# Optimization experiments

Hardware: AMD Instinct MI355X
Metric: run time of the kernel (lower is better)

Reference implementation:

```python
import jax, jax.numpy as jnp
import numpy as np

BITS = 4
GROUPSIZE = 128
INF = 4096
OUTF = 4096
PACK = 32 // BITS  # 8 nibbles per int32


def _dequant(qweight, qzeros, scales):
    # qweight: [INF//PACK, OUTF] int32, qzeros: [n_groups, OUTF//PACK] int32
    shifts = (jnp.arange(PACK, dtype=jnp.int32) * BITS)
    # unpack weights: each int32 row holds PACK consecutive input rows
    w = (qweight[:, None, :] >> shifts[None, :, None]) & 15        # [512, 8, 4096]
    w = w.reshape(-1, GROUPSIZE, OUTF)                              # [n_groups, groupsize, OUTF]
    # unpack zeros: each int32 col holds PACK consecutive output cols
    z = ((qzeros[:, :, None] >> shifts[None, None, :]) & 15) + 1   # [n_groups, 512, 8]
    z = z.reshape(z.shape[0], 1, -1)                                # [n_groups, 1, OUTF]
    W = scales[:, None, :] * (w - z).astype(scales.dtype)           # per-group dequant
    return W.reshape(INF, OUTF)


def setup_inputs() -> dict:
    key = jax.random.key(0)
    k1, k2, k3, k4, k5 = jax.random.split(key, 5)
    x = jax.random.normal(k1, (8, 512, INF), dtype=jnp.float32)
    qweight = jax.random.randint(k2, (INF // PACK, OUTF), 0, 2147483647, dtype=jnp.int32)
    n_groups = INF // GROUPSIZE
    qzeros = jax.random.randint(k3, (n_groups, OUTF // PACK), 0, 2147483647, dtype=jnp.int32)
    scales = jax.random.uniform(k4, (n_groups, OUTF), dtype=jnp.float32) * 0.01 + 0.001
    bias = jax.random.normal(k5, (OUTF,), dtype=jnp.float32) * 0.01
    return {"x": x, "qweight": qweight, "qzeros": qzeros, "scales": scales, "bias": bias}


def reference(x, qweight, qzeros, scales, bias):
    W = _dequant(qweight, qzeros, scales)        # [INF, OUTF] fp32
    out = jnp.matmul(x, W.astype(x.dtype)) + bias
    return out
```

## Files before the change

kernel.cpp:

```cpp
#include <hip/hip_runtime.h>
#include <hip/hip_bf16.h>


#define K_DIM 4096
#define N_DIM 4096
#define M_DIM 4096
#define BM 128
#define BN 128
#define BK 64
#define NGROUPS 32

typedef __attribute__((ext_vector_type(8))) short s8v;
typedef __attribute__((ext_vector_type(4))) float f4v;
typedef __attribute__((ext_vector_type(4))) unsigned int u4v;
typedef __attribute__((ext_vector_type(2))) unsigned int u2v;
typedef __attribute__((ext_vector_type(4))) float float4v;

typedef __attribute__((address_space(3))) void LDSV;
typedef const __attribute__((address_space(1))) void GLBV;

__device__ __forceinline__ void glds16(const void* g, void* l) {
    __builtin_amdgcn_global_load_lds((GLBV*)g, (LDSV*)l, 16, 0, 0);
}

__device__ __forceinline__ unsigned int bf16rne(float f) {
    unsigned int b = __float_as_uint(f);
    return (b + 0x7FFFu + ((b >> 16) & 1u)) >> 16;
}

__global__ __launch_bounds__(256) void castx(const float* __restrict__ x,
                                             unsigned short* __restrict__ xh,
                                             int n4) {
    int i0 = blockIdx.x * 256 + threadIdx.x;
    int st = gridDim.x * 256;
    for (int i = i0; i < n4; i += st) {
        float4v v = ((const float4v*)x)[i];
        unsigned int h[4];
#pragma unroll
        for (int j = 0; j < 4; j++) {
            unsigned int b = __float_as_uint(v[j]);
            h[j] = (b + 0x7FFFu + ((b >> 16) & 1u)) & 0xFFFF0000u;
        }
        u2v o = {(h[0] >> 16) | h[1], (h[2] >> 16) | h[3]};
        ((u2v*)xh)[i] = o;
    }
}

__global__ __launch_bounds__(256) void dequantW(const int* __restrict__ qw,
                                                const int* __restrict__ qz,
                                                const float* __restrict__ scales,
                                                unsigned short* __restrict__ wt) {
    __shared__ __align__(16) unsigned short T[256 * 64];
    const int b = blockIdx.x;
    const int kkb = b & 63;
    const int nb = b >> 6;
    const int tid = threadIdx.x;
    const int n = nb * 256 + tid;
    const int g = kkb >> 1;
    const float s = scales[g * N_DIM + n];
    const int zp1 = ((qz[g * 512 + (n >> 3)] >> ((n & 7) * 4)) & 15) + 1;

    char* Tb = (char*)T;
#pragma unroll
    for (int r = 0; r < 8; r++) {
        const unsigned int q = (unsigned int)qw[(kkb * 8 + r) * N_DIM + n];
        unsigned int hw[8];
#pragma unroll
        for (int j = 0; j < 8; j++) {
            float v = s * (float)((int)((q >> (4 * j)) & 15u) - zp1);
            hw[j] = bf16rne(v);
        }
        u4v d = {hw[0] | (hw[1] << 16), hw[2] | (hw[3] << 16),
                 hw[4] | (hw[5] << 16), hw[6] | (hw[7] << 16)};
        *(u4v*)(Tb + tid * 128 + ((r * 16) ^ ((tid & 7) << 4))) = d;
    }
    __syncthreads();
#pragma unroll
    for (int p = 0; p < 8; p++) {
        const int nl = p * 32 + (tid >> 3);
        const int c = tid & 7;
        u4v d = *(const u4v*)(Tb + nl * 128 + ((c * 16) ^ ((nl & 7) << 4)));
        *(u4v*)(wt + (size_t)(nb * 256 + nl) * K_DIM + kkb * 64 + c * 8) = d;
    }
}

__global__ __launch_bounds__(256, 2) void gemm_q4(
    const unsigned short* __restrict__ xh, const unsigned short* __restrict__ wt,
    const float* __restrict__ bias, float* __restrict__ out) {
    __shared__ __align__(16) unsigned short A[2][BM * BK];
    __shared__ __align__(16) unsigned short B[2][BN * BK];

    const int tid = threadIdx.x;
    const int lane = tid & 63;
    const int wid = tid >> 6;

    const int bid = blockIdx.x;
    const int wg = ((bid & 7) << 7) + (bid >> 3);
    const int bm = (wg >> 5) << 7;
    const int bn = (wg & 31) << 7;

    const int wr = ((wid >> 1) & 1) << 6;
    const int wc = (wid & 1) << 6;

    const f4v z4 = {0.f, 0.f, 0.f, 0.f};
    f4v acc[4][4];
#pragma unroll
    for (int i = 0; i < 4; i++)
#pragma unroll
        for (int j = 0; j < 4; j++) acc[i][j] = z4;

    const int arow = lane >> 3;
    const int aswz = ((lane & 7) ^ arow) << 3;
    const size_t a_gbase = (size_t)(bm + wid * 32 + arow) * K_DIM + aswz;
    const size_t b_gbase = (size_t)(bn + wid * 32 + arow) * K_DIM + aswz;

    const int frow = lane & 15;
    const int fk16 = (lane >> 4) << 4;
    const int row00 = bm + wr + ((lane >> 4) << 2);

    auto stage = [&](int kt, int b) {
        const unsigned short* ga = xh + a_gbase + kt * BK;
        const unsigned short* gb = wt + b_gbase + kt * BK;
        unsigned short* ad = &A[b][(wid * 32) * BK];
        unsigned short* bd = &B[b][(wid * 32) * BK];
#pragma unroll
        for (int i = 0; i < 4; i++) {
            glds16(ga + i * 8 * K_DIM, ad + i * 8 * BK);
            glds16(gb + i * 8 * K_DIM, bd + i * 8 * BK);
        }
    };
    auto compute = [&](int b) {
        const char* Ab = (const char*)&A[b][0];
        const char* Bb = (const char*)&B[b][0];
#pragma unroll
        for (int ks = 0; ks < 2; ks++) {
            const int kb = (ks << 6) | fk16;
            s8v bfr[4];
#pragma unroll
            for (int ni = 0; ni < 4; ni++) {
                const int r = wc + ni * 16 + frow;
                bfr[ni] = *(const s8v*)(Bb + r * 128 + (kb ^ ((r & 7) << 4)));
            }
#pragma unroll
            for (int mi = 0; mi < 4; mi++) {
                const int r = wr + mi * 16 + frow;
                s8v ah = *(const s8v*)(Ab + r * 128 + (kb ^ ((r & 7) << 4)));
#pragma unroll
                for (int ni = 0; ni < 4; ni++)
                    acc[mi][ni] = __builtin_amdgcn_mfma_f32_16x16x32_bf16(
                        ah, bfr[ni], acc[mi][ni], 0, 0, 0);
            }
        }
    };

    stage(0, 0);
    __syncthreads();

#pragma unroll 1
    for (int t = 0; t < 64; ++t) {
        if (t < 63) stage(t + 1, (t + 1) & 1);
        compute(t & 1);
        __syncthreads();
    }

    const int col0 = bn + wc + frow;
#pragma unroll
    for (int ni = 0; ni < 4; ni++) {
        const float bv = bias[col0 + ni * 16];
#pragma unroll
        for (int mi = 0; mi < 4; mi++) {
            f4v v = acc[mi][ni];
#pragma unroll
            for (int r2 = 0; r2 < 4; r2++)
                out[(size_t)(row00 + mi * 16 + r2) * N_DIM + col0 + ni * 16] =
                    v[r2] + bv;
        }
    }
}

__global__ __launch_bounds__(256) void naive_q4(
    const float* __restrict__ x, const int* __restrict__ qw,
    const int* __restrict__ qz, const float* __restrict__ scales,
    const float* __restrict__ bias, float* __restrict__ out) {
    const int n = (blockIdx.x & 63) * 64 + (threadIdx.x & 63);
    const int m = (blockIdx.x >> 6) * 4 + (threadIdx.x >> 6);
    const float* xr = x + (size_t)m * K_DIM;
    float acc = 0.f;
    for (int g = 0; g < NGROUPS; ++g) {
        const float s = scales[g * N_DIM + n];
        const int z = ((qz[g * 512 + (n >> 3)] >> ((n & 7) * 4)) & 15) + 1;
        float gs = 0.f;
        for (int kk = 0; kk < 16; ++kk) {
            const int q = qw[(g * 16 + kk) * N_DIM + n];
            const float* xp = xr + g * 128 + kk * 8;
#pragma unroll
            for (int j = 0; j < 8; j++)
                gs += xp[j] * (float)(((q >> (4 * j)) & 15) - z);
        }
        acc += s * gs;
    }
    out[(size_t)m * N_DIM + n] = acc + bias[n];
}

extern "C" void kernel_launch(void* const* d_in, const int* in_sizes, int n_in,
                              void* d_out, int out_size, void* d_ws,
                              size_t ws_size, hipStream_t stream) {
    const float* x = (const float*)d_in[0];
    const int* qw = (const int*)d_in[1];
    const int* qz = (const int*)d_in[2];
    const float* sc = (const float*)d_in[3];
    const float* bias = (const float*)d_in[4];
    float* out = (float*)d_out;

    const size_t nel = (size_t)M_DIM * K_DIM;
    const size_t need = nel * 2 * sizeof(unsigned short);
    if (ws_size >= need) {
        unsigned short* xh = (unsigned short*)d_ws;
        unsigned short* wtp = xh + nel;
        castx<<<2048, 256, 0, stream>>>(x, xh, (int)(nel / 4));
        dequantW<<<64 * 16, 256, 0, stream>>>(qw, qz, sc, wtp);
        gemm_q4<<<(M_DIM / BM) * (N_DIM / BN), 256, 0, stream>>>(xh, wtp, bias,
                                                                 out);
    } else {
        naive_q4<<<(M_DIM / 4) * (N_DIM / 64), 256, 0, stream>>>(x, qw, qz, sc,
                                                                 bias, out);
    }
}
```

Baseline: 272.3 us.

## Replace GEMM with 256x256-tile 8-wave kernel using fine-grained phased prefetch

The bf16 GEMM moves from 128x128 tiles with 4 waves to 256x256 tiles with 8 waves. Each wave now holds a 128x64 accumulator block. The K loop becomes eight phases per pair of K tiles, each interleaving half-tile global-to-LDS loads with MFMA work, using explicit vmcnt waits, barriers and setprio. This is meant to raise operand reuse per LDS byte and overlap memory traffic with compute more tightly. It uses more registers and 128KB of LDS per block, and it depends on the hand-tuned wait counts being correct.

```diff
diff --git a/kernel.cpp b/kernel.cpp
--- a/kernel.cpp
+++ b/kernel.cpp
@@ -5,8 +5,8 @@
 #define K_DIM 4096
 #define N_DIM 4096
 #define M_DIM 4096
-#define BM 128
-#define BN 128
+#define BM 256
+#define BN 256
 #define BK 64
 #define NGROUPS 32
 
@@ -84,96 +84,147 @@
     }
 }
 
-__global__ __launch_bounds__(256, 2) void gemm_q4(
+#define STAGE_A(BUF, H, T)                                                    \
+    {                                                                         \
+        _Pragma("unroll") for (int j = 0; j < 2; j++) {                       \
+            const int s_ = 2 * wid + j;                                       \
+            const int rA = (s_ < 8) ? ((H) * 64 + s_ * 8)                     \
+                                    : (128 + (H) * 64 + (s_ - 8) * 8);        \
+            glds16(xh + (size_t)(bm + rA + (lane >> 3)) * K_DIM + (T)*BK +    \
+                       aswz,                                                  \
+                   &LDS_[BUF][0][(H)*8192 + s_ * 512]);                       \
+        }                                                                     \
+    }
+#define STAGE_B(BUF, H, T)                                                    \
+    {                                                                         \
+        _Pragma("unroll") for (int j = 0; j < 2; j++) {                       \
+            const int s_ = 2 * wid + j;                                       \
+            const int cB = ((s_ >> 2) << 6) + ((H) << 5) + ((s_ & 3) << 3);   \
+            glds16(wt + (size_t)(bn + cB + (lane >> 3)) * K_DIM + (T)*BK +    \
+                       aswz,                                                  \
+                   &LDS_[BUF][1][(H)*8192 + s_ * 512]);                       \
+        }                                                                     \
+    }
+#define VM6 asm volatile("s_waitcnt vmcnt(6)" ::: "memory");
+#define VM0 asm volatile("s_waitcnt vmcnt(0)" ::: "memory");
+#define NOP ;
+
+#define PHASE(BUF, QM, QN, STAGE_CODE, WAIT_CODE)                             \
+    {                                                                         \
+        if ((QN) == 0) {                                                      \
+            const char* Ab = (const char*)&LDS_[BUF][0][(QM)*8192];           \
+            _Pragma("unroll") for (int mi = 0; mi < 4; mi++) {                \
+                const int pos = wr * 64 + mi * 16 + frow;                     \
+                const int ro = pos * 128;                                     \
+                const int sw = (pos & 7) << 4;                                \
+                afr[mi][0] = *(const s8v*)(Ab + ro + (fk16 ^ sw));            \
+                afr[mi][1] = *(const s8v*)(Ab + ro + ((64 | fk16) ^ sw));     \
+            }                                                                 \
+        }                                                                     \
+        if ((QM) == 0) {                                                      \
+            const char* Bb = (const char*)&LDS_[BUF][1][(QN)*8192];           \
+            _Pragma("unroll") for (int ni = 0; ni < 2; ni++) {                \
+                const int pos = wc * 32 + ni * 16 + frow;                     \
+                const int ro = pos * 128;                                     \
+                const int sw = (pos & 7) << 4;                                \
+                bfr[QN][ni][0] = *(const s8v*)(Bb + ro + (fk16 ^ sw));        \
+                bfr[QN][ni][1] = *(const s8v*)(Bb + ro + ((64 | fk16) ^ sw)); \
+            }                                                                 \
+        }                                                                     \
+        STAGE_CODE                                                            \
+        __builtin_amdgcn_s_barrier();                                         \
+        asm volatile("s_waitcnt lgkmcnt(0)" ::: "memory");                    \
+        __builtin_amdgcn_s_setprio(1);                                        \
+        _Pragma("unroll") for (int mi = 0; mi < 4; mi++)                      \
+            _Pragma("unroll") for (int ni = 0; ni < 2; ni++) {                \
+            acc[(QM)*4 + mi][(QN)*2 + ni] =                                   \
+                __builtin_amdgcn_mfma_f32_16x16x32_bf16(                      \
+                    afr[mi][0], bfr[QN][ni][0],                               \
+                    acc[(QM)*4 + mi][(QN)*2 + ni], 0, 0, 0);                  \
+            acc[(QM)*4 + mi][(QN)*2 + ni] =                                   \
+                __builtin_amdgcn_mfma_f32_16x16x32_bf16(                      \
+                    afr[mi][1], bfr[QN][ni][1],                               \
+                    acc[(QM)*4 + mi][(QN)*2 + ni], 0, 0, 0);                  \
+        }                                                                     \
+        __builtin_amdgcn_s_setprio(0);                                        \
+        WAIT_CODE                                                             \
+        __builtin_amdgcn_s_barrier();                                         \
+    }
+
+__global__ __launch_bounds__(512, 2) void gemm8(
     const unsigned short* __restrict__ xh, const unsigned short* __restrict__ wt,
     const float* __restrict__ bias, float* __restrict__ out) {
-    __shared__ __align__(16) unsigned short A[2][BM * BK];
-    __shared__ __align__(16) unsigned short B[2][BN * BK];
+    __shared__ __align__(16) unsigned short LDS_[2][2][16384];
 
     const int tid = threadIdx.x;
     const int lane = tid & 63;
     const int wid = tid >> 6;
+    const int wr = wid >> 2;
+    const int wc = wid & 3;
 
     const int bid = blockIdx.x;
-    const int wg = ((bid & 7) << 7) + (bid >> 3);
-    const int bm = (wg >> 5) << 7;
-    const int bn = (wg & 31) << 7;
-
-    const int wr = ((wid >> 1) & 1) << 6;
-    const int wc = (wid & 1) << 6;
-
-    const f4v z4 = {0.f, 0.f, 0.f, 0.f};
-    f4v acc[4][4];
-#pragma unroll
-    for (int i = 0; i < 4; i++)
-#pragma unroll
-        for (int j = 0; j < 4; j++) acc[i][j] = z4;
-
-    const int arow = lane >> 3;
-    const int aswz = ((lane & 7) ^ arow) << 3;
-    const size_t a_gbase = (size_t)(bm + wid * 32 + arow) * K_DIM + aswz;
-    const size_t b_gbase = (size_t)(bn + wid * 32 + arow) * K_DIM + aswz;
+    const int wg = ((bid & 7) << 5) + (bid >> 3);
+    const int bm = (wg >> 4) << 8;
+    const int bn = (wg & 15) << 8;
 
     const int frow = lane & 15;
     const int fk16 = (lane >> 4) << 4;
-    const int row00 = bm + wr + ((lane >> 4) << 2);
-
-    auto stage = [&](int kt, int b) {
-        const unsigned short* ga = xh + a_gbase + kt * BK;
-        const unsigned short* gb = wt + b_gbase + kt * BK;
-        unsigned short* ad = &A[b][(wid * 32) * BK];
-        unsigned short* bd = &B[b][(wid * 32) * BK];
-#pragma unroll
-        for (int i = 0; i < 4; i++) {
-            glds16(ga + i * 8 * K_DIM, ad + i * 8 * BK);
-            glds16(gb + i * 8 * K_DIM, bd + i * 8 * BK);
-        }
-    };
-    auto compute = [&](int b) {
-        const char* Ab = (const char*)&A[b][0];
-        const char* Bb = (const char*)&B[b][0];
-#pragma unroll
-        for (int ks = 0; ks < 2; ks++) {
-            const int kb = (ks << 6) | fk16;
-            s8v bfr[4];
-#pragma unroll
-            for (int ni = 0; ni < 4; ni++) {
-                const int r = wc + ni * 16 + frow;
-                bfr[ni] = *(const s8v*)(Bb + r * 128 + (kb ^ ((r & 7) << 4)));
-            }
-#pragma unroll
-            for (int mi = 0; mi < 4; mi++) {
-                const int r = wr + mi * 16 + frow;
-                s8v ah = *(const s8v*)(Ab + r * 128 + (kb ^ ((r & 7) << 4)));
-#pragma unroll
-                for (int ni = 0; ni < 4; ni++)
-                    acc[mi][ni] = __builtin_amdgcn_mfma_f32_16x16x32_bf16(
-                        ah, bfr[ni], acc[mi][ni], 0, 0, 0);
-            }
-        }
-    };
-
-    stage(0, 0);
-    __syncthreads();
+    const int aswz = ((lane & 7) ^ (lane >> 3)) << 3;
+
+    const f4v z4 = {0.f, 0.f, 0.f, 0.f};
+    f4v acc[8][4];
+#pragma unroll
+    for (int i = 0; i < 8; i++)
+#pragma unroll
+        for (int j = 0; j < 4; j++) acc[i][j] = z4;
+
+    s8v afr[4][2];
+    s8v bfr[2][2][2];
+
+    STAGE_A(0, 0, 0)
+    STAGE_A(0, 1, 0)
+    STAGE_B(0, 0, 0)
+    STAGE_B(0, 1, 0)
+    STAGE_A(1, 0, 1)
+    STAGE_B(1, 0, 1)
+    STAGE_B(1, 1, 1)
+    VM6
+    __builtin_amdgcn_s_barrier();
 
 #pragma unroll 1
-    for (int t = 0; t < 64; ++t) {
-        if (t < 63) stage(t + 1, (t + 1) & 1);
-        compute(t & 1);
-        __syncthreads();
-    }
-
-    const int col0 = bn + wc + frow;
-#pragma unroll
-    for (int ni = 0; ni < 4; ni++) {
-        const float bv = bias[col0 + ni * 16];
-#pragma unroll
-        for (int mi = 0; mi < 4; mi++) {
-            f4v v = acc[mi][ni];
+    for (int i = 0; i < 31; ++i) {
+        const int t1 = 2 * i + 1, t2 = 2 * i + 2, t3 = 2 * i + 3;
+        PHASE(0, 0, 0, STAGE_A(1, 1, t1), NOP)
+        PHASE(0, 0, 1, STAGE_A(0, 0, t2), NOP)
+        PHASE(0, 1, 0, STAGE_B(0, 0, t2), NOP)
+        PHASE(0, 1, 1, STAGE_B(0, 1, t2), VM6)
+        PHASE(1, 0, 0, STAGE_A(0, 1, t2), NOP)
+        PHASE(1, 0, 1, STAGE_A(1, 0, t3), NOP)
+        PHASE(1, 1, 0, STAGE_B(1, 0, t3), NOP)
+        PHASE(1, 1, 1, STAGE_B(1, 1, t3), VM6)
+    }
+    PHASE(0, 0, 0, STAGE_A(1, 1, 63), NOP)
+    PHASE(0, 0, 1, NOP, NOP)
+    PHASE(0, 1, 0, NOP, NOP)
+    PHASE(0, 1, 1, NOP, VM0)
+    PHASE(1, 0, 0, NOP, NOP)
+    PHASE(1, 0, 1, NOP, NOP)
+    PHASE(1, 1, 0, NOP, NOP)
+    PHASE(1, 1, 1, NOP, NOP)
+
+    const int row0 = bm + wr * 128 + ((lane >> 4) << 2);
+    const int col0 = bn + wc * 64 + frow;
+#pragma unroll
+    for (int n = 0; n < 4; n++) {
+        const int cn = col0 + (n >> 1) * 32 + (n & 1) * 16;
+        const float bv = bias[cn];
+#pragma unroll
+        for (int m = 0; m < 8; m++) {
+            const int rm = row0 + (m >> 2) * 64 + (m & 3) * 16;
+            f4v v = acc[m][n];
 #pragma unroll
             for (int r2 = 0; r2 < 4; r2++)
-                out[(size_t)(row00 + mi * 16 + r2) * N_DIM + col0 + ni * 16] =
-                    v[r2] + bv;
+                out[(size_t)(rm + r2) * N_DIM + cn] = v[r2] + bv;
         }
     }
 }
@@ -219,8 +270,8 @@
         unsigned short* wtp = xh + nel;
         castx<<<2048, 256, 0, stream>>>(x, xh, (int)(nel / 4));
         dequantW<<<64 * 16, 256, 0, stream>>>(qw, qz, sc, wtp);
-        gemm_q4<<<(M_DIM / BM) * (N_DIM / BN), 256, 0, stream>>>(xh, wtp, bias,
-                                                                 out);
+        gemm8<<<(M_DIM / BM) * (N_DIM / BN), 512, 0, stream>>>(xh, wtp, bias,
+                                                               out);
     } else {
         naive_q4<<<(M_DIM / 4) * (N_DIM / 64), 256, 0, stream>>>(x, qw, qz, sc,
                                                                  bias, out);
```

After: 248.4 us. 8.8% less time.
